# Optimization experiments

Measured on AMD Instinct MI355X. Metric: run time of the kernel, lower is better.

## Reference

```python
import jax, jax.numpy as jnp
import numpy as np

B, N, CIN, FOUT = 4, 512, 64, 64
EPS = 1e-5
NEG_SLOPE = 0.2


def setup_inputs() -> dict:
    key = jax.random.key(0)
    ks = jax.random.split(key, 10)
    s = lambda k, shape: (jax.random.normal(k, shape, dtype=jnp.float32) * 0.05)
    return {
        "x": jax.random.normal(ks[0], (B, N, CIN), dtype=jnp.float32),
        "adj": jax.random.uniform(ks[1], (N, N), dtype=jnp.float32),
        "W_w": s(ks[2], (FOUT, CIN)), "W_b": s(ks[3], (FOUT,)),
        "U_w": s(ks[4], (FOUT, FOUT)), "U_b": s(ks[5], (FOUT,)),
        "V_w": s(ks[6], (FOUT, FOUT)), "V_b": s(ks[7], (FOUT,)),
        "att_w": s(ks[8], (1, 2 * FOUT)), "att_b": s(ks[9], (1,)),
        "ln_g": jnp.ones((FOUT,), jnp.float32),
        "ln_b": jnp.zeros((FOUT,), jnp.float32),
    }


def reference(x, adj, W_w, W_b, U_w, U_b, V_w, V_b, att_w, att_b, ln_g, ln_b):
    # h = W(x): (B, N, F)
    h = x @ W_w.T + W_b
    Fd = h.shape[-1]
    # attention(cat[h_i, h_j]) == (h_i @ a_i) + (h_j @ a_j) + b  -> avoid (B,N,N,2F)
    a_i, a_j = att_w[0, :Fd], att_w[0, Fd:]
    logits = (h @ a_i)[:, :, None] + (h @ a_j)[:, None, :] + att_b[0]  # (B,N,N)
    logits = jnp.where(logits > 0, logits, NEG_SLOPE * logits)  # LeakyReLU(0.2)
    attn = jax.nn.softmax(logits, axis=-1)  # softmax over j; dropout is identity in eval
    # gate = sigmoid(U(h_i) + V(h_j)); U/V applied once per node then broadcast
    Uh = h @ U_w.T + U_b  # (B,N,F)
    Vh = h @ V_w.T + V_b  # (B,N,F)
    gate = jax.nn.sigmoid(Uh[:, :, None, :] + Vh[:, None, :, :])  # (B,N,N,F)
    node_features = gate * attn[..., None] * h[:, None, :, :]  # (B,N,N,F)
    # aggr[b,i,f] = sum_{j,k} nf[b,i,j,f] * adj[j,k]
    aggr = jnp.einsum('bijf,jk->bif', node_features, adj)
    # LayerNorm over last dim
    mu = jnp.mean(aggr, axis=-1, keepdims=True)
    var = jnp.var(aggr, axis=-1, keepdims=True)
    out = (aggr - mu) / jnp.sqrt(var + EPS) * ln_g + ln_b
    return out
```

## Files before the change

### kernel.cpp

```cpp
#include <hip/hip_runtime.h>

#define NB 4
#define NN 512
#define NF 64
#define NEG_SLOPE 0.2f
#define LN_EPS 1e-5f
#define JC 64

__device__ __forceinline__ float wave_sum(float v){
  #pragma unroll
  for (int d = 32; d; d >>= 1) v += __shfl_xor(v, d, 64);
  return v;
}
__device__ __forceinline__ float wave_max(float v){
  #pragma unroll
  for (int d = 32; d; d >>= 1) v = fmaxf(v, __shfl_xor(v, d, 64));
  return v;
}


extern "C" __global__ __launch_bounds__(64)
void k_setup(const float* __restrict__ x, const float* __restrict__ adj,
             const float* __restrict__ Ww, const float* __restrict__ Wb,
             const float* __restrict__ Uw, const float* __restrict__ Ub,
             const float* __restrict__ Vw, const float* __restrict__ Vb,
             const float* __restrict__ attw,
             float* __restrict__ ws)
{
  float* r   = ws;
  float* evh = ws + NN;
  float* eU  = evh + NB*NN*NF*2;
  float* li  = eU + NB*NN*NF;
  float* lj  = li + NB*NN;

  const int blk  = blockIdx.x;
  const int lane = threadIdx.x;

  if (blk >= NB*NN) {
    int j = blk - NB*NN;
    const float2* a2 = (const float2*)(adj + j*NN);
    float s = 0.f;
    #pragma unroll
    for (int t = 0; t < 4; t++){
      float2 a = a2[lane + 64*t];
      s += a.x + a.y;
    }
    s = wave_sum(s);
    if (lane == 0) r[j] = s;
    return;
  }

  const int row = blk;
  __shared__ float sx[NF];
  __shared__ float sh[NF];

  sx[lane] = x[row*NF + lane];
  __syncthreads();

  float hv = Wb[lane];
  {
    const float4* w4 = (const float4*)(Ww + lane*NF);
    #pragma unroll
    for (int t = 0; t < 16; t++){
      float4 w = w4[t];
      hv = fmaf(sx[4*t+0], w.x, hv);
      hv = fmaf(sx[4*t+1], w.y, hv);
      hv = fmaf(sx[4*t+2], w.z, hv);
      hv = fmaf(sx[4*t+3], w.w, hv);
    }
  }
  sh[lane] = hv;
  __syncthreads();

  float uh = Ub[lane];
  float vh = Vb[lane];
  {
    const float4* u4 = (const float4*)(Uw + lane*NF);
    const float4* v4 = (const float4*)(Vw + lane*NF);
    #pragma unroll
    for (int t = 0; t < 16; t++){
      float4 uu = u4[t]; float4 vv = v4[t];
      float h0 = sh[4*t+0], h1 = sh[4*t+1], h2 = sh[4*t+2], h3 = sh[4*t+3];
      uh = fmaf(h0, uu.x, uh); vh = fmaf(h0, vv.x, vh);
      uh = fmaf(h1, uu.y, uh); vh = fmaf(h1, vv.y, vh);
      uh = fmaf(h2, uu.z, uh); vh = fmaf(h2, vv.z, vh);
      uh = fmaf(h3, uu.w, uh); vh = fmaf(h3, vv.w, vh);
    }
  }

  float ev = __expf(-vh);
  float eu = __expf(-uh);
  ((float2*)evh)[row*NF + lane] = make_float2(ev, hv);
  eU[row*NF + lane] = eu;

  float pi = wave_sum(hv * attw[lane]);
  float pj = wave_sum(hv * attw[NF + lane]);
  if (lane == 0){ li[row] = pi; lj[row] = pj; }
}

extern "C" __global__ __launch_bounds__(256)
void k_main(const float* __restrict__ attb_p,
            const float* __restrict__ lng,
            const float* __restrict__ lnb,
            const float* __restrict__ ws,
            float* __restrict__ out)
{
  const float* r   = ws;
  const float* evh = ws + NN;
  const float* eU  = evh + NB*NN*NF*2;
  const float* li  = eU + NB*NN*NF;
  const float* lj  = li + NB*NN;

  __shared__ float s_c[4][NN];
  __shared__ float s_evh[JC*NF*2];

  const int tid  = threadIdx.x;
  const int w    = tid >> 6;
  const int lane = tid & 63;
  const int b    = blockIdx.x >> 7;
  const int i    = (blockIdx.x & 127)*4 + w;

  const float attb = attb_p[0];
  const float li_s = li[b*NN + i];

  float lv[8];
  float m = -1e30f;
  #pragma unroll
  for (int t = 0; t < 8; t++){
    int j = lane + 64*t;
    float l = li_s + lj[b*NN + j] + attb;
    l = (l > 0.f) ? l : NEG_SLOPE*l;
    lv[t] = l;
    m = fmaxf(m, l);
  }
  m = wave_max(m);
  float S = 0.f;
  #pragma unroll
  for (int t = 0; t < 8; t++){ lv[t] = __expf(lv[t] - m); S += lv[t]; }
  S = wave_sum(S);
  float inv = __builtin_amdgcn_rcpf(S);
  #pragma unroll
  for (int t = 0; t < 8; t++){
    int j = lane + 64*t;
    s_c[w][j] = lv[t]*inv*r[j];
  }

  const float eu = eU[(b*NN + i)*NF + lane];
  float acc = 0.f;
  __syncthreads();

  for (int c0 = 0; c0 < NN; c0 += JC){
    const float4* g4 = (const float4*)(evh + (b*NN + c0)*NF*2);
    float4* s4 = (float4*)s_evh;
    #pragma unroll
    for (int t = 0; t < (JC*NF*2/4)/256; t++){
      s4[tid + t*256] = g4[tid + t*256];
    }
    __syncthreads();
    const float2* sevh2 = (const float2*)s_evh;
    #pragma unroll 8
    for (int jj = 0; jj < JC; jj++){
      float cj = s_c[w][c0 + jj];
      float2 eh = sevh2[jj*NF + lane];
      float q = fmaf(eu, eh.x, 1.0f);
      acc = fmaf(cj, eh.y * __builtin_amdgcn_rcpf(q), acc);
    }
    __syncthreads();
  }

  float s1 = wave_sum(acc);
  float s2 = wave_sum(acc*acc);
  float mu  = s1 * (1.f/NF);
  float var = s2 * (1.f/NF) - mu*mu;
  float rs  = __builtin_amdgcn_rsqf(var + LN_EPS);
  float o = (acc - mu)*rs*lng[lane] + lnb[lane];
  out[(b*NN + i)*NF + lane] = o;
}

extern "C" void kernel_launch(void* const* d_in, const int* in_sizes, int n_in,
                              void* d_out, int out_size, void* d_ws, size_t ws_size,
                              hipStream_t stream)
{
  const float* x    = (const float*)d_in[0];
  const float* adj  = (const float*)d_in[1];
  const float* Ww   = (const float*)d_in[2];
  const float* Wb   = (const float*)d_in[3];
  const float* Uw   = (const float*)d_in[4];
  const float* Ub   = (const float*)d_in[5];
  const float* Vw   = (const float*)d_in[6];
  const float* Vb   = (const float*)d_in[7];
  const float* attw = (const float*)d_in[8];
  const float* attb = (const float*)d_in[9];
  const float* lng  = (const float*)d_in[10];
  const float* lnb  = (const float*)d_in[11];
  float* ws = (float*)d_ws;
  float* outp = (float*)d_out;

  hipLaunchKernelGGL(k_setup, dim3(NB*NN + NN), dim3(64), 0, stream,
                     x, adj, Ww, Wb, Uw, Ub, Vw, Vb, attw, ws);
  hipLaunchKernelGGL(k_main, dim3(NB*NN/4), dim3(256), 0, stream,
                     attb, lng, lnb, ws, outp);
}
```

Before: 104.8 us.

## Split j range across waves, reuse each evh load for four rows

Each wave now covers a quarter of the j range and computes partial sums for all four rows i of the block, so one global load of (exp(-V), h) feeds four rows. The shared-memory staging of evh chunks and the per-chunk barriers go away, and partial accumulators are combined through a small shared buffer. The attention coefficients are stored j-major so one float4 read gives all four rows' weights. This cuts global/LDS traffic per useful FLOP, at the cost of more registers and direct uncached-in-LDS global loads.

```diff
diff --git a/kernel.cpp b/kernel.cpp
--- a/kernel.cpp
+++ b/kernel.cpp
@@ -5,7 +5,6 @@
 #define NF 64
 #define NEG_SLOPE 0.2f
 #define LN_EPS 1e-5f
-#define JC 64
 
 __device__ __forceinline__ float wave_sum(float v){
   #pragma unroll
@@ -111,14 +110,15 @@
   const float* li  = eU + NB*NN*NF;
   const float* lj  = li + NB*NN;
 
-  __shared__ float s_c[4][NN];
-  __shared__ float s_evh[JC*NF*2];
+  __shared__ float s_c[NN][4];
+  __shared__ float s_part[4][4][NF];
 
   const int tid  = threadIdx.x;
   const int w    = tid >> 6;
   const int lane = tid & 63;
   const int b    = blockIdx.x >> 7;
-  const int i    = (blockIdx.x & 127)*4 + w;
+  const int i0   = (blockIdx.x & 127) * 4;
+  const int i    = i0 + w;
 
   const float attb = attb_p[0];
   const float li_s = li[b*NN + i];
@@ -142,31 +142,42 @@
   #pragma unroll
   for (int t = 0; t < 8; t++){
     int j = lane + 64*t;
-    s_c[w][j] = lv[t]*inv*r[j];
-  }
-
-  const float eu = eU[(b*NN + i)*NF + lane];
-  float acc = 0.f;
-  __syncthreads();
-
-  for (int c0 = 0; c0 < NN; c0 += JC){
-    const float4* g4 = (const float4*)(evh + (b*NN + c0)*NF*2);
-    float4* s4 = (float4*)s_evh;
-    #pragma unroll
-    for (int t = 0; t < (JC*NF*2/4)/256; t++){
-      s4[tid + t*256] = g4[tid + t*256];
-    }
-    __syncthreads();
-    const float2* sevh2 = (const float2*)s_evh;
-    #pragma unroll 8
-    for (int jj = 0; jj < JC; jj++){
-      float cj = s_c[w][c0 + jj];
-      float2 eh = sevh2[jj*NF + lane];
-      float q = fmaf(eu, eh.x, 1.0f);
-      acc = fmaf(cj, eh.y * __builtin_amdgcn_rcpf(q), acc);
-    }
-    __syncthreads();
-  }
+    s_c[j][w] = lv[t]*inv*r[j];
+  }
+
+  const float eu0 = eU[(b*NN + i0 + 0)*NF + lane];
+  const float eu1 = eU[(b*NN + i0 + 1)*NF + lane];
+  const float eu2 = eU[(b*NN + i0 + 2)*NF + lane];
+  const float eu3 = eU[(b*NN + i0 + 3)*NF + lane];
+
+  __syncthreads();
+
+  const float2* evh2 = (const float2*)evh + (size_t)(b*NN)*NF;
+  float a0 = 0.f, a1 = 0.f, a2 = 0.f, a3 = 0.f;
+  const int j0 = w*128;
+  #pragma unroll 8
+  for (int jj = 0; jj < 128; jj++){
+    int j = j0 + jj;
+    float2 eh = evh2[j*NF + lane];
+    float4 c4 = *(const float4*)&s_c[j][0];
+    float q0 = fmaf(eu0, eh.x, 1.0f);
+    float q1 = fmaf(eu1, eh.x, 1.0f);
+    float q2 = fmaf(eu2, eh.x, 1.0f);
+    float q3 = fmaf(eu3, eh.x, 1.0f);
+    a0 = fmaf(c4.x, eh.y * __builtin_amdgcn_rcpf(q0), a0);
+    a1 = fmaf(c4.y, eh.y * __builtin_amdgcn_rcpf(q1), a1);
+    a2 = fmaf(c4.z, eh.y * __builtin_amdgcn_rcpf(q2), a2);
+    a3 = fmaf(c4.w, eh.y * __builtin_amdgcn_rcpf(q3), a3);
+  }
+
+  s_part[w][0][lane] = a0;
+  s_part[w][1][lane] = a1;
+  s_part[w][2][lane] = a2;
+  s_part[w][3][lane] = a3;
+  __syncthreads();
+
+  float acc = s_part[0][w][lane] + s_part[1][w][lane]
+            + s_part[2][w][lane] + s_part[3][w][lane];
 
   float s1 = wave_sum(acc);
   float s2 = wave_sum(acc*acc);
```

New measurement: 103.7 us. No clear change (-1.1%).
